# Optimization experiments

Measured on AMD Instinct MI355X. Metric: run time of the kernel, lower is better.

Reference implementation:

```python
import jax, jax.numpy as jnp
import numpy as np


def _row_forward(rows, W1, b1, W_ih, W_hh, b_ih, b_hh, W3, b3):
    """Batched version of the per-row pipeline: fc1 -> ReLU -> 1-step LSTM (zero init
    state) -> ReLU -> fc3 -> softmax. rows: [N, input_size]."""
    h1 = jax.nn.relu(rows @ W1.T + b1)              # [N, 256]
    # LSTM single step with h0 = c0 = 0: the W_hh @ h0 term vanishes.
    gates = h1 @ W_ih.T + (b_ih + b_hh)             # [N, 4*H2], gate order i,f,g,o
    i, f, g, o = jnp.split(gates, 4, axis=-1)
    c = jax.nn.sigmoid(i) * jnp.tanh(g)             # c = i*g since c0 = 0 (f gate unused)
    h = jax.nn.sigmoid(o) * jnp.tanh(c)             # [N, H2]
    h = jax.nn.relu(h)
    return jax.nn.softmax(h @ W3.T + b3, axis=-1)   # [N, num_classes]


def setup_inputs() -> dict:
    key = jax.random.key(0)
    ks = jax.random.split(key, 9)
    P, M, A, B = 64, 16, 512, 128       # patients, mats/patient, input_size, rows/mat
    H1, H2, C = 256, 256, 32            # hidden1 (hardcoded 256 in view), hidden2, classes
    def w(k, shape, fan):
        return (jax.random.normal(k, shape, jnp.float32) / np.float32(np.sqrt(fan)))
    return {
        "x": jax.random.normal(ks[0], (P, M, A, B), jnp.float32),
        "W1": w(ks[1], (H1, A), A), "b1": w(ks[2], (H1,), A),
        "W_ih": w(ks[3], (4 * H2, H1), H1), "W_hh": w(ks[4], (4 * H2, H2), H2),
        "b_ih": w(ks[5], (4 * H2,), H1), "b_hh": w(ks[6], (4 * H2,), H1),
        "W3": w(ks[7], (C, H2), H2), "b3": w(ks[8], (C,), H2),
    }


def reference(x, W1, b1, W_ih, W_hh, b_ih, b_hh, W3, b3):
    P, M, A, B = x.shape
    # Original iterates rows of mat.transpose(1,0) (i.e. columns of mat). Every row is
    # an independent evaluation because the LSTM hidden state is reset (None) per row,
    # so we batch all P*M*B rows into one fused pipeline.
    rows = x.transpose(0, 1, 3, 2).reshape(P * M * B, A)
    outs = _row_forward(rows, W1, b1, W_ih, W_hh, b_ih, b_hh, W3, b3)  # [P*M*B, C]
    outs = outs.reshape(P, M * B, -1)
    # cumOut keeps only the result of the LAST row of the LAST mat per patient.
    return outs[:, -1, :]  # [P, num_classes]
```

## Files before the change

kernel.cpp:

```cpp
#include <hip/hip_runtime.h>
#include <cmath>

#define NP 64
#define NM 16
#define NA 512
#define NB 128
#define H1 256
#define H2 256
#define NC 32

__device__ __forceinline__ float sigmoid_(float x) {
    return 1.0f / (1.0f + __expf(-x));
}

extern "C" __global__ __launch_bounds__(256)
void rnn_fused(const float* __restrict__ x,
               const float* __restrict__ W1, const float* __restrict__ b1,
               const float* __restrict__ W_ih,
               const float* __restrict__ b_ih, const float* __restrict__ b_hh,
               const float* __restrict__ W3, const float* __restrict__ b3,
               float* __restrict__ out)
{
    __shared__ float row[NA];
    __shared__ float h1s[H1];
    __shared__ float hs[H2];
    __shared__ float logits[NC];

    const int p = blockIdx.x;
    const int t = threadIdx.x;

    const size_t abase = ((size_t)p * NM + (NM - 1)) * NA;
    for (int a = t; a < NA; a += 256)
        row[a] = x[(abase + a) * NB + (NB - 1)];
    __syncthreads();

    {
        const float4* w = (const float4*)(W1 + (size_t)t * NA);
        const float4* r = (const float4*)row;
        float acc = 0.f;
        #pragma unroll 8
        for (int k = 0; k < NA / 4; ++k) {
            float4 wv = w[k], rv = r[k];
            acc = fmaf(wv.x, rv.x, acc);
            acc = fmaf(wv.y, rv.y, acc);
            acc = fmaf(wv.z, rv.z, acc);
            acc = fmaf(wv.w, rv.w, acc);
        }
        h1s[t] = fmaxf(acc + b1[t], 0.f);
    }
    __syncthreads();

    {
        float ai = b_ih[t]            + b_hh[t];
        float ag = b_ih[2 * H2 + t]   + b_hh[2 * H2 + t];
        float ao = b_ih[3 * H2 + t]   + b_hh[3 * H2 + t];
        const float4* wi = (const float4*)(W_ih + (size_t)t * H1);
        const float4* wg = (const float4*)(W_ih + (size_t)(2 * H2 + t) * H1);
        const float4* wo = (const float4*)(W_ih + (size_t)(3 * H2 + t) * H1);
        const float4* hv = (const float4*)h1s;
        #pragma unroll 8
        for (int k = 0; k < H1 / 4; ++k) {
            float4 h4 = hv[k];
            float4 a4 = wi[k];
            float4 g4 = wg[k];
            float4 o4 = wo[k];
            ai = fmaf(a4.x, h4.x, fmaf(a4.y, h4.y, fmaf(a4.z, h4.z, fmaf(a4.w, h4.w, ai))));
            ag = fmaf(g4.x, h4.x, fmaf(g4.y, h4.y, fmaf(g4.z, h4.z, fmaf(g4.w, h4.w, ag))));
            ao = fmaf(o4.x, h4.x, fmaf(o4.y, h4.y, fmaf(o4.z, h4.z, fmaf(o4.w, h4.w, ao))));
        }
        float c = sigmoid_(ai) * tanhf(ag);
        float h = sigmoid_(ao) * tanhf(c);
        hs[t] = fmaxf(h, 0.f);
    }
    __syncthreads();

    {
        const int g = t >> 3;
        const int l = t & 7;
        const float4* w  = (const float4*)(W3 + (size_t)g * H2);
        const float4* hv = (const float4*)hs;
        float acc = 0.f;
        #pragma unroll
        for (int j = 0; j < 8; ++j) {
            float4 wv = w[l + 8 * j];
            float4 h4 = hv[l + 8 * j];
            acc = fmaf(wv.x, h4.x, acc);
            acc = fmaf(wv.y, h4.y, acc);
            acc = fmaf(wv.z, h4.z, acc);
            acc = fmaf(wv.w, h4.w, acc);
        }
        acc += __shfl_down(acc, 4, 64);
        acc += __shfl_down(acc, 2, 64);
        acc += __shfl_down(acc, 1, 64);
        if (l == 0) logits[g] = acc + b3[g];
    }
    __syncthreads();

    if (t < NC) {
        float v = logits[t];
        float m = v;
        #pragma unroll
        for (int off = 16; off; off >>= 1) m = fmaxf(m, __shfl_xor(m, off, 64));
        float e = __expf(v - m);
        float s = e;
        #pragma unroll
        for (int off = 16; off; off >>= 1) s += __shfl_xor(s, off, 64);
        out[p * NC + t] = e / s;
    }
}

extern "C" void kernel_launch(void* const* d_in, const int* in_sizes, int n_in,
                              void* d_out, int out_size, void* d_ws, size_t ws_size,
                              hipStream_t stream) {
    const float* x    = (const float*)d_in[0];
    const float* W1   = (const float*)d_in[1];
    const float* b1   = (const float*)d_in[2];
    const float* W_ih = (const float*)d_in[3];
    const float* b_ih = (const float*)d_in[5];
    const float* b_hh = (const float*)d_in[6];
    const float* W3   = (const float*)d_in[7];
    const float* b3   = (const float*)d_in[8];
    float* out = (float*)d_out;

    hipLaunchKernelGGL(rnn_fused, dim3(NP), dim3(256), 0, stream,
                       x, W1, b1, W_ih, b_ih, b_hh, W3, b3, out);
}
```

Before: 42.76 us.

## Split fused per-patient kernel into three batched kernels sharing weights across patients

The single fused kernel, with one block per patient that reads all the weights, is replaced by three kernels. fc1 tiles 8 patients by 32 outputs per block, the LSTM kernel gives each block 4 hidden units across all 64 patients, and fc3 with softmax runs per patient. Intermediate activations go through workspace memory. The aim is to cut redundant weight traffic: before, every block streamed the full W1 and three quarters of W_ih. The cost is two extra launches plus global round-trips, and the LSTM kernel now reads h1 with strided per-thread loads.

```diff
diff --git a/kernel.cpp b/kernel.cpp
--- a/kernel.cpp
+++ b/kernel.cpp
@@ -13,87 +13,108 @@
     return 1.0f / (1.0f + __expf(-x));
 }
 
+__device__ __forceinline__ float dot4(float4 a, float4 b, float acc) {
+    acc = fmaf(a.x, b.x, acc);
+    acc = fmaf(a.y, b.y, acc);
+    acc = fmaf(a.z, b.z, acc);
+    acc = fmaf(a.w, b.w, acc);
+    return acc;
+}
+
 extern "C" __global__ __launch_bounds__(256)
-void rnn_fused(const float* __restrict__ x,
-               const float* __restrict__ W1, const float* __restrict__ b1,
-               const float* __restrict__ W_ih,
-               const float* __restrict__ b_ih, const float* __restrict__ b_hh,
-               const float* __restrict__ W3, const float* __restrict__ b3,
-               float* __restrict__ out)
+void k1_fc1(const float* __restrict__ x,
+            const float* __restrict__ W1, const float* __restrict__ b1,
+            float* __restrict__ h1out)
 {
-    __shared__ float row[NA];
-    __shared__ float h1s[H1];
-    __shared__ float hs[H2];
+    __shared__ float rows[8][NA];
+
+    const int pt = blockIdx.x >> 3;
+    const int ot = blockIdx.x & 7;
+    const int t  = threadIdx.x;
+
+    for (int idx = t; idx < 8 * NA; idx += 256) {
+        const int pl = idx >> 9;
+        const int a  = idx & (NA - 1);
+        const size_t gi = ((((size_t)(pt * 8 + pl) * NM + (NM - 1)) * NA + a) * NB) + (NB - 1);
+        rows[pl][a] = x[gi];
+    }
+    __syncthreads();
+
+    const int pl = t >> 5;
+    const int ol = t & 31;
+    const int o  = ot * 32 + ol;
+
+    const float4* w = (const float4*)(W1 + (size_t)o * NA);
+    const float4* r = (const float4*)rows[pl];
+
+    float a0 = 0.f, a1 = 0.f, a2 = 0.f, a3 = 0.f;
+    #pragma unroll 8
+    for (int k = 0; k < NA / 4; k += 4) {
+        a0 = dot4(w[k + 0], r[k + 0], a0);
+        a1 = dot4(w[k + 1], r[k + 1], a1);
+        a2 = dot4(w[k + 2], r[k + 2], a2);
+        a3 = dot4(w[k + 3], r[k + 3], a3);
+    }
+    const float v = (a0 + a1) + (a2 + a3) + b1[o];
+    h1out[(size_t)(pt * 8 + pl) * H1 + o] = fmaxf(v, 0.f);
+}
+
+extern "C" __global__ __launch_bounds__(256)
+void k2_lstm(const float* __restrict__ h1in,
+             const float* __restrict__ W_ih,
+             const float* __restrict__ b_ih, const float* __restrict__ b_hh,
+             float* __restrict__ hout)
+{
+    const int t = threadIdx.x;
+    const int j = blockIdx.x * 4 + (t >> 6);
+    const int p = t & 63;
+
+    const float4* wi = (const float4*)(W_ih + (size_t)j * H1);
+    const float4* wg = (const float4*)(W_ih + (size_t)(2 * H2 + j) * H1);
+    const float4* wo = (const float4*)(W_ih + (size_t)(3 * H2 + j) * H1);
+    const float4* hv = (const float4*)(h1in + (size_t)p * H1);
+
+    float i0 = 0.f, i1 = 0.f, g0 = 0.f, g1 = 0.f, o0 = 0.f, o1 = 0.f;
+    #pragma unroll 8
+    for (int k = 0; k < H1 / 4; k += 2) {
+        float4 h4a = hv[k], h4b = hv[k + 1];
+        i0 = dot4(wi[k], h4a, i0);  i1 = dot4(wi[k + 1], h4b, i1);
+        g0 = dot4(wg[k], h4a, g0);  g1 = dot4(wg[k + 1], h4b, g1);
+        o0 = dot4(wo[k], h4a, o0);  o1 = dot4(wo[k + 1], h4b, o1);
+    }
+    const float ai = i0 + i1 + b_ih[j]            + b_hh[j];
+    const float ag = g0 + g1 + b_ih[2 * H2 + j]   + b_hh[2 * H2 + j];
+    const float ao = o0 + o1 + b_ih[3 * H2 + j]   + b_hh[3 * H2 + j];
+
+    const float c = sigmoid_(ai) * tanhf(ag);
+    const float h = sigmoid_(ao) * tanhf(c);
+    hout[(size_t)p * H2 + j] = fmaxf(h, 0.f);
+}
+
+extern "C" __global__ __launch_bounds__(256)
+void k3_fc3(const float* __restrict__ hin,
+            const float* __restrict__ W3, const float* __restrict__ b3,
+            float* __restrict__ out)
+{
     __shared__ float logits[NC];
 
     const int p = blockIdx.x;
     const int t = threadIdx.x;
 
-    const size_t abase = ((size_t)p * NM + (NM - 1)) * NA;
-    for (int a = t; a < NA; a += 256)
-        row[a] = x[(abase + a) * NB + (NB - 1)];
-    __syncthreads();
+    const int g = t >> 3;
+    const int l = t & 7;
 
-    {
-        const float4* w = (const float4*)(W1 + (size_t)t * NA);
-        const float4* r = (const float4*)row;
-        float acc = 0.f;
-        #pragma unroll 8
-        for (int k = 0; k < NA / 4; ++k) {
-            float4 wv = w[k], rv = r[k];
-            acc = fmaf(wv.x, rv.x, acc);
-            acc = fmaf(wv.y, rv.y, acc);
-            acc = fmaf(wv.z, rv.z, acc);
-            acc = fmaf(wv.w, rv.w, acc);
-        }
-        h1s[t] = fmaxf(acc + b1[t], 0.f);
-    }
-    __syncthreads();
+    const float4* w  = (const float4*)(W3 + (size_t)g * H2);
+    const float4* hv = (const float4*)(hin + (size_t)p * H2);
+    float acc = 0.f;
+    #pragma unroll
+    for (int j = 0; j < 8; ++j)
+        acc = dot4(w[l + 8 * j], hv[l + 8 * j], acc);
 
-    {
-        float ai = b_ih[t]            + b_hh[t];
-        float ag = b_ih[2 * H2 + t]   + b_hh[2 * H2 + t];
-        float ao = b_ih[3 * H2 + t]   + b_hh[3 * H2 + t];
-        const float4* wi = (const float4*)(W_ih + (size_t)t * H1);
-        const float4* wg = (const float4*)(W_ih + (size_t)(2 * H2 + t) * H1);
-        const float4* wo = (const float4*)(W_ih + (size_t)(3 * H2 + t) * H1);
-        const float4* hv = (const float4*)h1s;
-        #pragma unroll 8
-        for (int k = 0; k < H1 / 4; ++k) {
-            float4 h4 = hv[k];
-            float4 a4 = wi[k];
-            float4 g4 = wg[k];
-            float4 o4 = wo[k];
-            ai = fmaf(a4.x, h4.x, fmaf(a4.y, h4.y, fmaf(a4.z, h4.z, fmaf(a4.w, h4.w, ai))));
-            ag = fmaf(g4.x, h4.x, fmaf(g4.y, h4.y, fmaf(g4.z, h4.z, fmaf(g4.w, h4.w, ag))));
-            ao = fmaf(o4.x, h4.x, fmaf(o4.y, h4.y, fmaf(o4.z, h4.z, fmaf(o4.w, h4.w, ao))));
-        }
-        float c = sigmoid_(ai) * tanhf(ag);
-        float h = sigmoid_(ao) * tanhf(c);
-        hs[t] = fmaxf(h, 0.f);
-    }
-    __syncthreads();
-
-    {
-        const int g = t >> 3;
-        const int l = t & 7;
-        const float4* w  = (const float4*)(W3 + (size_t)g * H2);
-        const float4* hv = (const float4*)hs;
-        float acc = 0.f;
-        #pragma unroll
-        for (int j = 0; j < 8; ++j) {
-            float4 wv = w[l + 8 * j];
-            float4 h4 = hv[l + 8 * j];
-            acc = fmaf(wv.x, h4.x, acc);
-            acc = fmaf(wv.y, h4.y, acc);
-            acc = fmaf(wv.z, h4.z, acc);
-            acc = fmaf(wv.w, h4.w, acc);
-        }
-        acc += __shfl_down(acc, 4, 64);
-        acc += __shfl_down(acc, 2, 64);
-        acc += __shfl_down(acc, 1, 64);
-        if (l == 0) logits[g] = acc + b3[g];
-    }
+    acc += __shfl_down(acc, 4, 64);
+    acc += __shfl_down(acc, 2, 64);
+    acc += __shfl_down(acc, 1, 64);
+    if (l == 0) logits[g] = acc + b3[g];
     __syncthreads();
 
     if (t < NC) {
@@ -122,6 +143,10 @@
     const float* b3   = (const float*)d_in[8];
     float* out = (float*)d_out;
 
-    hipLaunchKernelGGL(rnn_fused, dim3(NP), dim3(256), 0, stream,
-                       x, W1, b1, W_ih, b_ih, b_hh, W3, b3, out);
+    float* h1 = (float*)d_ws;
+    float* h  = h1 + (size_t)NP * H1;
+
+    hipLaunchKernelGGL(k1_fc1, dim3(64), dim3(256), 0, stream, x, W1, b1, h1);
+    hipLaunchKernelGGL(k2_lstm, dim3(64), dim3(256), 0, stream, h1, W_ih, b_ih, b_hh, h);
+    hipLaunchKernelGGL(k3_fc3, dim3(64), dim3(256), 0, stream, h, W3, b3, out);
 }
```

New measurement: 43.88 us. 2.6% more time.
